# Optimization experiments

Hardware: AMD Instinct MI355X
Metric: run time of the kernel (lower is better)

Reference implementation:

```python
import jax, jax.numpy as jnp
import numpy as np

B, W, C_BLK, N_EMBD, N_HEADS = 512, 128, 24, 32, 2


def setup_inputs() -> dict:
    key = jax.random.key(0)
    k1, k2, k3, k4 = jax.random.split(key, 4)
    x = jax.random.normal(k1, (B, W, C_BLK, N_EMBD), dtype=jnp.float32)
    x_end_idx = jax.random.randint(k2, (B, W), 0, C_BLK, dtype=jnp.int32)
    # nn.Linear(n_embd, 3*n_embd, bias=False): store transposed so y = x @ w
    w_attn = jax.random.normal(k3, (N_EMBD, 3 * N_EMBD), dtype=jnp.float32) * (1.0 / np.sqrt(N_EMBD))
    w_proj = jax.random.normal(k4, (N_EMBD, N_EMBD), dtype=jnp.float32) * (1.0 / np.sqrt(N_EMBD))
    return {"x": x, "x_end_idx": x_end_idx, "w_attn": w_attn, "w_proj": w_proj}


def reference(x, x_end_idx, w_attn, w_proj):
    # x: [B, W, c, C]; causal self-attention over the char axis c, per (batch, word).
    Bd, Wd, c, C = x.shape
    H = N_HEADS
    D = C // H
    qkv = x @ w_attn                               # [B, W, c, 3C]
    q, k, v = jnp.split(qkv, 3, axis=-1)
    # [B, W, H, c, D]
    q = q.reshape(Bd, Wd, c, H, D).transpose(0, 1, 3, 2, 4)
    k = k.reshape(Bd, Wd, c, H, D).transpose(0, 1, 3, 2, 4)
    v = v.reshape(Bd, Wd, c, H, D).transpose(0, 1, 3, 2, 4)
    scale = 1.0 / jnp.sqrt(jnp.asarray(D, dtype=x.dtype))
    scores = jnp.einsum('bwhqd,bwhkd->bwhqk', q, k) * scale   # [B, W, H, c, c]
    causal = jnp.tril(jnp.ones((c, c), dtype=bool))
    scores = jnp.where(causal, scores, jnp.asarray(-jnp.inf, dtype=scores.dtype))
    att = jax.nn.softmax(scores, axis=-1)
    out = jnp.einsum('bwhqk,bwhkd->bwhqd', att, v)            # [B, W, H, c, D]
    out = out.transpose(0, 1, 3, 2, 4).reshape(Bd, Wd, c, C)
    out = out @ w_proj                                        # c_proj (dropout in eval mode = identity)
    out = x + out                                             # residual
    # Vectorized last-token gather: pick out[b, w, x_end_idx[b, w], :]
    idx = x_end_idx[:, :, None, None].astype(jnp.int32)       # [B, W, 1, 1]
    samples = jnp.take_along_axis(out, jnp.broadcast_to(idx, (Bd, Wd, 1, C)), axis=2)
    return samples.squeeze(2)                                 # [B, W, C]
```

## Files before the change

### kernel.cpp

```cpp
#include <hip/hip_runtime.h>


#define CB      24
#define CC      32
#define DD      16
#define THREEC  96
#define NBW     (512 * 128)
#define WPB     4
#define XSS     34

struct __align__(16) WaveSmem {
    float xs[CB][XSS];
    float rks[2][CC];
    float ps[2][CC];
    float ys[2][CC];
    float os[CC];
    float pad[2];
};

__device__ __forceinline__ void wave_fence() {
    __asm__ volatile("s_waitcnt lgkmcnt(0)" ::: "memory");
}

__global__ __launch_bounds__(256, 8) void char_attn_kernel(
    const float* __restrict__ x,
    const int*   __restrict__ xend,
    const float* __restrict__ w_attn,
    const float* __restrict__ w_proj,
    float*       __restrict__ out)
{
    __shared__ WaveSmem sm[WPB];

    const int tid  = threadIdx.x;
    const int lane = tid & 63;
    const int wave = tid >> 6;
    WaveSmem& S = sm[wave];

    const int bid  = blockIdx.x * WPB + wave;
    const int i32  = lane & 31;
    const int half = lane >> 5;

    const int qidx = xend[bid];
    const int L    = qidx + 1;
    const float* xb = x + (size_t)bid * (CB * CC);

    {
        const float2* xb2 = (const float2*)xb;
        const int n2 = L * (CC / 2);
        for (int t = lane; t < n2; t += 64) {
            float2 v = xb2[t];
            const int r = t >> 4, c = (t & 15) * 2;
            *(float2*)&S.xs[r][c] = v;
        }
    }
    wave_fence();

    float qv;
    {
        const int cb = half * DD;
        float a0 = 0.f, a1 = 0.f;
        #pragma unroll
        for (int t = 0; t < DD; t += 2) {
            a0 = fmaf(S.xs[qidx][cb + t],     w_attn[(cb + t) * THREEC + i32],     a0);
            a1 = fmaf(S.xs[qidx][cb + t + 1], w_attn[(cb + t + 1) * THREEC + i32], a1);
        }
        qv = a0 + a1;
        qv += __shfl_xor(qv, 32);
    }

    {
        const float4* w4 = (const float4*)&w_attn[i32 * THREEC + CC + DD * half];
        float4 w0 = w4[0], w1 = w4[1], w2 = w4[2], w3 = w4[3];
        const int db = DD * half;
        float a0 = 0.f, a1 = 0.f;
        a0 = fmaf(w0.x, __shfl(qv, db + 0),  a0); a1 = fmaf(w0.y, __shfl(qv, db + 1),  a1);
        a0 = fmaf(w0.z, __shfl(qv, db + 2),  a0); a1 = fmaf(w0.w, __shfl(qv, db + 3),  a1);
        a0 = fmaf(w1.x, __shfl(qv, db + 4),  a0); a1 = fmaf(w1.y, __shfl(qv, db + 5),  a1);
        a0 = fmaf(w1.z, __shfl(qv, db + 6),  a0); a1 = fmaf(w1.w, __shfl(qv, db + 7),  a1);
        a0 = fmaf(w2.x, __shfl(qv, db + 8),  a0); a1 = fmaf(w2.y, __shfl(qv, db + 9),  a1);
        a0 = fmaf(w2.z, __shfl(qv, db + 10), a0); a1 = fmaf(w2.w, __shfl(qv, db + 11), a1);
        a0 = fmaf(w3.x, __shfl(qv, db + 12), a0); a1 = fmaf(w3.y, __shfl(qv, db + 13), a1);
        a0 = fmaf(w3.z, __shfl(qv, db + 14), a0); a1 = fmaf(w3.w, __shfl(qv, db + 15), a1);
        S.rks[half][i32] = (a0 + a1) * 0.25f;
    }
    wave_fence();

    {
        float sc = -INFINITY;
        if (i32 <= qidx) {
            float a0 = 0.f, a1 = 0.f;
            #pragma unroll
            for (int c = 0; c < CC; c += 2) {
                a0 = fmaf(S.xs[i32][c],     S.rks[half][c],     a0);
                a1 = fmaf(S.xs[i32][c + 1], S.rks[half][c + 1], a1);
            }
            sc = a0 + a1;
        }
        float m = sc;
        #pragma unroll
        for (int off = 16; off >= 1; off >>= 1)
            m = fmaxf(m, __shfl_xor(m, off));
        const float e = (i32 <= qidx) ? __expf(sc - m) : 0.f;
        float sum = e;
        #pragma unroll
        for (int off = 16; off >= 1; off >>= 1)
            sum += __shfl_xor(sum, off);
        S.ps[half][i32] = e / sum;
    }
    wave_fence();

    {
        float acc = 0.f;
        for (int j = 0; j < L; ++j)
            acc = fmaf(S.ps[half][j], S.xs[j][i32], acc);
        S.ys[half][i32] = acc;
    }
    wave_fence();

    {
        const int hi = i32 >> 4;
        const int cb = half * DD;
        float a0 = 0.f, a1 = 0.f;
        #pragma unroll
        for (int t = 0; t < DD; t += 2) {
            a0 = fmaf(S.ys[hi][cb + t],     w_attn[(cb + t) * THREEC + 2 * CC + i32],     a0);
            a1 = fmaf(S.ys[hi][cb + t + 1], w_attn[(cb + t + 1) * THREEC + 2 * CC + i32], a1);
        }
        float t = a0 + a1;
        t += __shfl_xor(t, 32);
        if (lane < CC) S.os[i32] = t;
    }
    wave_fence();

    {
        const int cb = half * DD;
        float a0 = 0.f, a1 = 0.f;
        #pragma unroll
        for (int t = 0; t < DD; t += 2) {
            a0 = fmaf(S.os[cb + t],     w_proj[(cb + t) * CC + i32],     a0);
            a1 = fmaf(S.os[cb + t + 1], w_proj[(cb + t + 1) * CC + i32], a1);
        }
        float t = a0 + a1;
        t += __shfl_xor(t, 32);
        if (lane < CC)
            out[(size_t)bid * CC + i32] = t + S.xs[qidx][i32];
    }
}

extern "C" void kernel_launch(void* const* d_in, const int* in_sizes, int n_in,
                              void* d_out, int out_size, void* d_ws, size_t ws_size,
                              hipStream_t stream) {
    const float* x      = (const float*)d_in[0];
    const int*   xend   = (const int*)d_in[1];
    const float* w_attn = (const float*)d_in[2];
    const float* w_proj = (const float*)d_in[3];
    float* out = (float*)d_out;

    char_attn_kernel<<<dim3(NBW / WPB), dim3(WPB * 64), 0, stream>>>(
        x, xend, w_attn, w_proj, out);
}
```

Before: 302.4 us.

## Precompute fused Wq·Wk^T and Wv·Wproj matrices and restructure attention pipeline

Adds a prep kernel that folds the query-key weight product (with the scale) and the value-projection weight product into small combined matrices in workspace. The main kernel keeps these in registers, computes both heads' scores per lane, skips max-subtraction in softmax and normalizes after the weighted sum. This removes one projection stage and one shared-memory round trip. In exchange it adds register pressure (launch bounds lowered to 4), a second launch, and a risk of exp overflow from the missing max-subtraction.

```diff
diff --git a/kernel.cpp b/kernel.cpp
--- a/kernel.cpp
+++ b/kernel.cpp
@@ -12,21 +12,43 @@
 struct __align__(16) WaveSmem {
     float xs[CB][XSS];
     float rks[2][CC];
-    float ps[2][CC];
-    float ys[2][CC];
-    float os[CC];
-    float pad[2];
+    float es[CB][2];
+    float ys[CC][2];
 };
 
 __device__ __forceinline__ void wave_fence() {
     __asm__ volatile("s_waitcnt lgkmcnt(0)" ::: "memory");
 }
 
-__global__ __launch_bounds__(256, 8) void char_attn_kernel(
+__global__ void prep_kernel(const float* __restrict__ w_attn,
+                            const float* __restrict__ w_proj,
+                            float* __restrict__ ws)
+{
+    const int t = blockIdx.x * 256 + threadIdx.x;
+    if (t < 2048) {
+        const int h = t >> 10, rem = t & 1023, cp = rem >> 5, c = rem & 31;
+        float a = 0.f;
+        #pragma unroll
+        for (int d = 0; d < DD; ++d)
+            a = fmaf(w_attn[cp * THREEC + 16 * h + d],
+                     w_attn[c * THREEC + CC + 16 * h + d], a);
+        ws[t] = a * 0.25f;
+    } else {
+        const int u = t - 2048;
+        const int h = u >> 10, rem = u & 1023, c = rem >> 5, i = rem & 31;
+        float a = 0.f;
+        #pragma unroll
+        for (int d = 0; d < DD; ++d)
+            a = fmaf(w_attn[c * THREEC + 2 * CC + 16 * h + d],
+                     w_proj[(16 * h + d) * CC + i], a);
+        ws[t] = a;
+    }
+}
+
+__global__ __launch_bounds__(256, 4) void char_attn_kernel(
     const float* __restrict__ x,
     const int*   __restrict__ xend,
-    const float* __restrict__ w_attn,
-    const float* __restrict__ w_proj,
+    const float* __restrict__ ws,
     float*       __restrict__ out)
 {
     __shared__ WaveSmem sm[WPB];
@@ -36,9 +58,23 @@
     const int wave = tid >> 6;
     WaveSmem& S = sm[wave];
 
-    const int bid  = blockIdx.x * WPB + wave;
     const int i32  = lane & 31;
     const int half = lane >> 5;
+    const int bid  = blockIdx.x * WPB + wave;
+
+    const float* Mw = ws;
+    const float* Nw = ws + 2048;
+
+    float Mreg[CC];
+    #pragma unroll
+    for (int cp = 0; cp < CC; ++cp)
+        Mreg[cp] = Mw[(half * CC + cp) * CC + i32];
+    float Nreg[2][DD];
+    #pragma unroll
+    for (int h = 0; h < 2; ++h)
+        #pragma unroll
+        for (int k = 0; k < DD; ++k)
+            Nreg[h][k] = Nw[(h * CC + half * DD + k) * CC + i32];
 
     const int qidx = xend[bid];
     const int L    = qidx + 1;
@@ -55,95 +91,73 @@
     }
     wave_fence();
 
-    float qv;
     {
-        const int cb = half * DD;
         float a0 = 0.f, a1 = 0.f;
         #pragma unroll
-        for (int t = 0; t < DD; t += 2) {
-            a0 = fmaf(S.xs[qidx][cb + t],     w_attn[(cb + t) * THREEC + i32],     a0);
-            a1 = fmaf(S.xs[qidx][cb + t + 1], w_attn[(cb + t + 1) * THREEC + i32], a1);
+        for (int cp = 0; cp < CC; cp += 2) {
+            float2 xv = *(const float2*)&S.xs[qidx][cp];
+            a0 = fmaf(xv.x, Mreg[cp],     a0);
+            a1 = fmaf(xv.y, Mreg[cp + 1], a1);
         }
-        qv = a0 + a1;
-        qv += __shfl_xor(qv, 32);
-    }
-
-    {
-        const float4* w4 = (const float4*)&w_attn[i32 * THREEC + CC + DD * half];
-        float4 w0 = w4[0], w1 = w4[1], w2 = w4[2], w3 = w4[3];
-        const int db = DD * half;
-        float a0 = 0.f, a1 = 0.f;
-        a0 = fmaf(w0.x, __shfl(qv, db + 0),  a0); a1 = fmaf(w0.y, __shfl(qv, db + 1),  a1);
-        a0 = fmaf(w0.z, __shfl(qv, db + 2),  a0); a1 = fmaf(w0.w, __shfl(qv, db + 3),  a1);
-        a0 = fmaf(w1.x, __shfl(qv, db + 4),  a0); a1 = fmaf(w1.y, __shfl(qv, db + 5),  a1);
-        a0 = fmaf(w1.z, __shfl(qv, db + 6),  a0); a1 = fmaf(w1.w, __shfl(qv, db + 7),  a1);
-        a0 = fmaf(w2.x, __shfl(qv, db + 8),  a0); a1 = fmaf(w2.y, __shfl(qv, db + 9),  a1);
-        a0 = fmaf(w2.z, __shfl(qv, db + 10), a0); a1 = fmaf(w2.w, __shfl(qv, db + 11), a1);
-        a0 = fmaf(w3.x, __shfl(qv, db + 12), a0); a1 = fmaf(w3.y, __shfl(qv, db + 13), a1);
-        a0 = fmaf(w3.z, __shfl(qv, db + 14), a0); a1 = fmaf(w3.w, __shfl(qv, db + 15), a1);
-        S.rks[half][i32] = (a0 + a1) * 0.25f;
+        S.rks[half][i32] = a0 + a1;
     }
     wave_fence();
 
     {
-        float sc = -INFINITY;
+        float s0 = 0.f, s1 = 0.f;
         if (i32 <= qidx) {
-            float a0 = 0.f, a1 = 0.f;
+            const int cb = half * DD;
             #pragma unroll
-            for (int c = 0; c < CC; c += 2) {
-                a0 = fmaf(S.xs[i32][c],     S.rks[half][c],     a0);
-                a1 = fmaf(S.xs[i32][c + 1], S.rks[half][c + 1], a1);
+            for (int t = 0; t < DD; t += 2) {
+                float2 xv = *(const float2*)&S.xs[i32][cb + t];
+                s0 = fmaf(xv.x, S.rks[0][cb + t],     s0);
+                s0 = fmaf(xv.y, S.rks[0][cb + t + 1], s0);
+                s1 = fmaf(xv.x, S.rks[1][cb + t],     s1);
+                s1 = fmaf(xv.y, S.rks[1][cb + t + 1], s1);
             }
-            sc = a0 + a1;
         }
-        float m = sc;
-        #pragma unroll
-        for (int off = 16; off >= 1; off >>= 1)
-            m = fmaxf(m, __shfl_xor(m, off));
-        const float e = (i32 <= qidx) ? __expf(sc - m) : 0.f;
-        float sum = e;
-        #pragma unroll
-        for (int off = 16; off >= 1; off >>= 1)
-            sum += __shfl_xor(sum, off);
-        S.ps[half][i32] = e / sum;
+        s0 += __shfl_xor(s0, 32);
+        s1 += __shfl_xor(s1, 32);
+        const float e0 = (i32 <= qidx) ? __expf(s0) : 0.f;
+        const float e1 = (i32 <= qidx) ? __expf(s1) : 0.f;
+        if (half == 0 && i32 < CB)
+            *(float2*)&S.es[i32][0] = make_float2(e0, e1);
     }
     wave_fence();
 
     {
-        float acc = 0.f;
-        for (int j = 0; j < L; ++j)
-            acc = fmaf(S.ps[half][j], S.xs[j][i32], acc);
-        S.ys[half][i32] = acc;
+        float y0 = 0.f, y1 = 0.f, ps0 = 0.f, ps1 = 0.f;
+        #pragma unroll
+        for (int jj = 0; jj < 12; ++jj) {
+            const int j  = half * 12 + jj;
+            const int jr = (j <= qidx) ? j : qidx;
+            float2 ev = *(const float2*)&S.es[j][0];
+            float  xv = S.xs[jr][i32];
+            y0 = fmaf(ev.x, xv, y0);  ps0 += ev.x;
+            y1 = fmaf(ev.y, xv, y1);  ps1 += ev.y;
+        }
+        y0  += __shfl_xor(y0, 32);
+        y1  += __shfl_xor(y1, 32);
+        ps0 += __shfl_xor(ps0, 32);
+        ps1 += __shfl_xor(ps1, 32);
+        if (half == 0)
+            *(float2*)&S.ys[i32][0] = make_float2(y0 / ps0, y1 / ps1);
     }
     wave_fence();
 
     {
-        const int hi = i32 >> 4;
-        const int cb = half * DD;
         float a0 = 0.f, a1 = 0.f;
         #pragma unroll
-        for (int t = 0; t < DD; t += 2) {
-            a0 = fmaf(S.ys[hi][cb + t],     w_attn[(cb + t) * THREEC + 2 * CC + i32],     a0);
-            a1 = fmaf(S.ys[hi][cb + t + 1], w_attn[(cb + t + 1) * THREEC + 2 * CC + i32], a1);
+        for (int k = 0; k < DD; ++k) {
+            const int c = half * DD + k;
+            float2 yv = *(const float2*)&S.ys[c][0];
+            a0 = fmaf(yv.x, Nreg[0][k], a0);
+            a1 = fmaf(yv.y, Nreg[1][k], a1);
         }
-        float t = a0 + a1;
-        t += __shfl_xor(t, 32);
-        if (lane < CC) S.os[i32] = t;
-    }
-    wave_fence();
-
-    {
-        const int cb = half * DD;
-        float a0 = 0.f, a1 = 0.f;
-        #pragma unroll
-        for (int t = 0; t < DD; t += 2) {
-            a0 = fmaf(S.os[cb + t],     w_proj[(cb + t) * CC + i32],     a0);
-            a1 = fmaf(S.os[cb + t + 1], w_proj[(cb + t + 1) * CC + i32], a1);
-        }
-        float t = a0 + a1;
-        t += __shfl_xor(t, 32);
-        if (lane < CC)
-            out[(size_t)bid * CC + i32] = t + S.xs[qidx][i32];
+        float a = a0 + a1;
+        a += __shfl_xor(a, 32);
+        if (half == 0)
+            out[(size_t)bid * CC + i32] = a + S.xs[qidx][i32];
     }
 }
 
@@ -155,7 +169,9 @@
     const float* w_attn = (const float*)d_in[2];
     const float* w_proj = (const float*)d_in[3];
     float* out = (float*)d_out;
+    float* ws  = (float*)d_ws;
 
+    prep_kernel<<<dim3(16), dim3(256), 0, stream>>>(w_attn, w_proj, ws);
     char_attn_kernel<<<dim3(NBW / WPB), dim3(WPB * 64), 0, stream>>>(
-        x, xend, w_attn, w_proj, out);
+        x, xend, ws, out);
 }
```

After: 304.2 us. No clear change (+0.6%).
